# Kernel optimization log

Hardware: AMD Instinct MI355X
Metric: run time of the kernel (lower is better)

The kernel has to match this reference:

```python
import jax, jax.numpy as jnp
import numpy as np

B, C, H, W = 16, 256, 64, 64
LDCE, CDCE = 100, 128


def _conv(x, w, groups=1):
    # x: NCHW, w: OIHW, stride 1, SAME padding (matches pad=1 for 3x3, pad=0 for 1x1)
    return jax.lax.conv_general_dilated(x, w, (1, 1), 'SAME',
                                        feature_group_count=groups,
                                        dimension_numbers=('NCHW', 'OIHW', 'NCHW'))


def _bn(x, g, b, eps=1e-5):
    # training-mode BatchNorm2d: biased batch stats over (N,H,W)
    m = jnp.mean(x, axis=(0, 2, 3), keepdims=True)
    v = jnp.var(x, axis=(0, 2, 3), keepdims=True)
    return g[None, :, None, None] * (x - m) * jax.lax.rsqrt(v + eps) + b[None, :, None, None]


def _silu(z):
    return z * jax.nn.sigmoid(z)


def setup_inputs() -> dict:
    key = jax.random.key(0)
    ks = jax.random.split(key, 18)
    f32 = jnp.float32
    s = 0.05
    d = {}
    d['x'] = jax.random.normal(ks[0], (B, C, H, W), f32)
    d['dce_output'] = jax.random.normal(ks[1], (B, LDCE, CDCE), f32)
    # DCE projection Linear(dce_dim -> out_feat)
    d['w_dce'] = jax.random.normal(ks[2], (C, CDCE), f32) * s
    d['b_dce'] = jax.random.normal(ks[3], (C,), f32) * s
    # per-channel 3x3 convs, stacked as a depthwise kernel (C,1,3,3)
    d['w_ch'] = jax.random.normal(ks[4], (C, 1, 3, 3), f32) * s
    # shrink / expand MLP
    d['w_shrink'] = jax.random.normal(ks[5], (C // 2, C), f32) * s
    d['b_shrink'] = jax.random.normal(ks[6], (C // 2,), f32) * s
    d['w_expand'] = jax.random.normal(ks[7], (C, C // 2), f32) * s
    d['b_expand'] = jax.random.normal(ks[8], (C,), f32) * s
    # ResBlock backbone: conv3x3 -> BN -> SiLU -> conv1x1 -> BN
    d['w_conv1'] = jax.random.normal(ks[9], (C, C, 3, 3), f32) * s
    d['g_bn1'] = jnp.ones((C,), f32)
    d['be_bn1'] = jnp.zeros((C,), f32)
    d['w_conv2'] = jax.random.normal(ks[10], (C, C, 1, 1), f32) * s
    d['g_bn2'] = jnp.ones((C,), f32)
    d['be_bn2'] = jnp.zeros((C,), f32)
    # shortcut: conv1x1 -> BN
    d['w_sc'] = jax.random.normal(ks[11], (C, C, 1, 1), f32) * s
    d['g_bns'] = jnp.ones((C,), f32)
    d['be_bns'] = jnp.zeros((C,), f32)
    return d


def reference(x, dce_output, w_dce, b_dce, w_ch, w_shrink, b_shrink,
              w_expand, b_expand, w_conv1, g_bn1, be_bn1, w_conv2, g_bn2,
              be_bn2, w_sc, g_bns, be_bns):
    C2 = w_dce.shape[0]
    # 1. AdaptiveAvgPool1d(1) over sequence, then Linear: (B, C2)
    dce_pooled = jnp.mean(dce_output, axis=1)            # (B, CDCE)
    dce_proj = dce_pooled @ w_dce.T + b_dce              # (B, C2)
    # 2. per-channel Conv2d(1,1,3) + global avg pool == depthwise conv + mean
    conv_out = _conv(x, w_ch, groups=C2)                 # (B, C2, H, W)
    spatial_proj = jnp.mean(conv_out, axis=(2, 3))       # (B, C2)
    # 3-5. modulation gate
    m = dce_proj * spatial_proj
    h = jax.nn.relu(m @ w_shrink.T + b_shrink)
    mod = jax.nn.sigmoid(h @ w_expand.T + b_expand)      # (B, C2)
    # 6. channel-wise modulation
    xm = x * mod[:, :, None, None]
    # 7. ResBlock
    bb = _silu(_bn(_conv(xm, w_conv1), g_bn1, be_bn1))
    bb = _bn(_conv(bb, w_conv2), g_bn2, be_bn2)
    sc = _bn(_conv(xm, w_sc), g_bns, be_bns)
    return _silu(bb + sc)
```

## Files before the change

kernel.cpp:

```cpp
#include <hip/hip_runtime.h>

typedef unsigned short u16;
typedef unsigned int   u32;
typedef __attribute__((ext_vector_type(8))) __bf16 bf16x8;
typedef __attribute__((ext_vector_type(4))) float  f32x4;

#define HW 4096
#define NPOS 65536
#define CH 256
#define MT 512
#define NMT 256

__device__ __forceinline__ u16 f2bf(float f){
  u32 u = __float_as_uint(f);
  u += 0x7FFFu + ((u >> 16) & 1u);
  return (u16)(u >> 16);
}
__device__ __forceinline__ float bflo(u32 p){ return __uint_as_float(p << 16); }
__device__ __forceinline__ float bfhi(u32 p){ return __uint_as_float(p & 0xFFFF0000u); }

#define GLL16(g, l) __builtin_amdgcn_global_load_lds( \
    (__attribute__((address_space(1))) void*)(g), \
    (__attribute__((address_space(3))) void*)(l), 16, 0, 0)

#define VM4() asm volatile("s_waitcnt vmcnt(4)" ::: "memory")
#define VM0() asm volatile("s_waitcnt vmcnt(0)" ::: "memory")
#define BARX() do { __builtin_amdgcn_s_barrier(); __builtin_amdgcn_sched_barrier(0); } while(0)
#define SP1() __builtin_amdgcn_s_setprio(1)
#define SP0() __builtin_amdgcn_s_setprio(0)

#define MMQ(Aa, Bb, IO, JO) \
  { _Pragma("unroll") for (int fi=0; fi<4; fi++){ \
      _Pragma("unroll") for (int fj=0; fj<2; fj++){ \
        acc[(IO)+fi][(JO)+fj] = __builtin_amdgcn_mfma_f32_16x16x32_bf16(Aa[0][fi], Bb[0][fj], acc[(IO)+fi][(JO)+fj], 0,0,0); \
        acc[(IO)+fi][(JO)+fj] = __builtin_amdgcn_mfma_f32_16x16x32_bf16(Aa[1][fi], Bb[1][fj], acc[(IO)+fi][(JO)+fj], 0,0,0); \
  } } }

#define RDA(dst, D, QOFF) \
  { _Pragma("unroll") for (int fi=0; fi<4; fi++){ \
      dst[0][fi] = *(const bf16x8*)&SH[(D) + aBase + (QOFF) + fi*1024 + kx0]; \
      dst[1][fi] = *(const bf16x8*)&SH[(D) + aBase + (QOFF) + fi*1024 + kx1]; \
  } }
#define RDB(dst, D, JOFF) \
  { _Pragma("unroll") for (int fj=0; fj<2; fj++){ \
      dst[0][fj] = *(const bf16x8*)&SH[(D) + bBase + (JOFF) + fj*1024 + kx0]; \
      dst[1][fj] = *(const bf16x8*)&SH[(D) + bBase + (JOFF) + fj*1024 + kx1]; \
  } }

__global__ __launch_bounds__(256) void k_statsx(const float* __restrict__ x, float* __restrict__ stats){
  int bc = blockIdx.x; int tid = threadIdx.x;
  const float* xp = x + (size_t)bc * HW;
  float S=0.f, r0=0.f, r1=0.f, c0=0.f, c1=0.f;
  #pragma unroll
  for (int k=0;k<4;k++){
    int i4 = tid + k*256;
    float4 v = ((const float4*)xp)[i4];
    int pos = i4*4; int h = pos>>6; int wb = pos&63;
    float sv = v.x+v.y+v.z+v.w;
    S += sv;
    if (h==0)  r0 += sv;
    if (h==63) r1 += sv;
    if (wb==0)  c0 += v.x;
    if (wb==60) c1 += v.w;
  }
  __shared__ float red[4][5];
  #pragma unroll
  for (int off=32; off>0; off>>=1){
    S  += __shfl_down(S, off);
    r0 += __shfl_down(r0, off);
    r1 += __shfl_down(r1, off);
    c0 += __shfl_down(c0, off);
    c1 += __shfl_down(c1, off);
  }
  if ((tid & 63) == 0){
    int w = tid >> 6;
    red[w][0]=S; red[w][1]=r0; red[w][2]=r1; red[w][3]=c0; red[w][4]=c1;
  }
  __syncthreads();
  if (tid == 0){
    float* o = stats + (size_t)bc * 9;
    for (int j=0;j<5;j++) o[j] = red[0][j]+red[1][j]+red[2][j]+red[3][j];
    o[5] = xp[0];
    o[6] = xp[63];
    o[7] = xp[4032];
    o[8] = xp[4095];
  }
}

__global__ __launch_bounds__(256) void k_gate(const float* __restrict__ dce,
    const float* __restrict__ stats, const float* __restrict__ wch,
    const float* __restrict__ w_dce, const float* __restrict__ b_dce,
    const float* __restrict__ w_sh, const float* __restrict__ b_sh,
    const float* __restrict__ w_ex, const float* __restrict__ b_ex,
    float* __restrict__ modb){
  int b = blockIdx.x, tid = threadIdx.x;
  __shared__ float pl[128];
  __shared__ float mbuf[256];
  __shared__ float hbuf[128];
  __shared__ float ptmp[256];
  {
    int k = tid & 127, half = tid >> 7;
    const float* p = dce + (size_t)b*12800 + half*50*128 + k;
    float s = 0.f;
    #pragma unroll 5
    for (int l=0;l<50;l++) s += p[l*128];
    ptmp[tid] = s;
  }
  __syncthreads();
  if (tid < 128) pl[tid] = (ptmp[tid] + ptmp[tid+128]) * 0.01f;
  __syncthreads();
  {
    int c = tid;
    const float* st = stats + (size_t)(b*256+c)*9;
    float S=st[0], r0=st[1], r1=st[2], cc0=st[3], cc1=st[4];
    float x00=st[5], x0W=st[6], xH0=st[7], xHW=st[8];
    float acc = 0.f;
    #pragma unroll
    for (int t=0;t<9;t++){
      int dh = t/3 - 1, dw = t%3 - 1;
      float R = (dh==1)? r0 : (dh==-1)? r1 : 0.f;
      float Cc = (dw==1)? cc0 : (dw==-1)? cc1 : 0.f;
      float X = 0.f;
      if (dh==1 && dw==1) X = x00;
      else if (dh==1 && dw==-1) X = x0W;
      else if (dh==-1 && dw==1) X = xH0;
      else if (dh==-1 && dw==-1) X = xHW;
      acc += wch[c*9+t] * (S - R - Cc + X);
    }
    float sp_ = acc * (1.f/4096.f);
    float dp = b_dce[c];
    const float4* wr = (const float4*)(w_dce + c*128);
    #pragma unroll 8
    for (int k4=0;k4<32;k4++){
      float4 w4 = wr[k4];
      dp += w4.x*pl[k4*4] + w4.y*pl[k4*4+1] + w4.z*pl[k4*4+2] + w4.w*pl[k4*4+3];
    }
    mbuf[c] = sp_ * dp;
  }
  __syncthreads();
  if (tid < 128){
    int j = tid;
    float acc = b_sh[j];
    const float4* wr = (const float4*)(w_sh + j*256);
    #pragma unroll 8
    for (int k4=0;k4<64;k4++){
      float4 w4 = wr[k4];
      acc += w4.x*mbuf[k4*4] + w4.y*mbuf[k4*4+1] + w4.z*mbuf[k4*4+2] + w4.w*mbuf[k4*4+3];
    }
    hbuf[j] = fmaxf(acc, 0.f);
  }
  __syncthreads();
  {
    int c = tid;
    float acc = b_ex[c];
    const float4* wr = (const float4*)(w_ex + c*128);
    #pragma unroll 8
    for (int k4=0;k4<32;k4++){
      float4 w4 = wr[k4];
      acc += w4.x*hbuf[k4*4] + w4.y*hbuf[k4*4+1] + w4.z*hbuf[k4*4+2] + w4.w*hbuf[k4*4+3];
    }
    modb[b*256+c] = 1.f/(1.f + __expf(-acc));
  }
}

__global__ __launch_bounds__(256) void k_wprep(const float* __restrict__ w1,
    const float* __restrict__ wsc, const float* __restrict__ w2,
    u16* __restrict__ w1t, u16* __restrict__ wsct, u16* __restrict__ w2t){
  int bx = blockIdx.x, ci = threadIdx.x;
  if (bx < 2304){
    int co = bx / 9, t = bx - co*9;
    w1t[(size_t)co*2304 + t*256 + ci] = f2bf(w1[(size_t)(co*256+ci)*9 + t]);
  } else if (bx < 2560){
    int i = (bx-2304)*256 + ci;
    wsct[i] = f2bf(wsc[i]);
  } else {
    int i = (bx-2560)*256 + ci;
    w2t[i] = f2bf(w2[i]);
  }
}

__global__ __launch_bounds__(256) void k_xm(const float* __restrict__ x, const float* __restrict__ modb,
                                            u16* __restrict__ xm){
  __shared__ __attribute__((aligned(16))) u16 tile[64*266];
  int pt = blockIdx.x, ct = blockIdx.y, tid = threadIdx.x;
  size_t P0 = (size_t)pt * 256;
  int b = pt >> 4;
  int rem = (pt & 15) << 8;
  int C0 = ct << 6;
  {
    int c = tid >> 2, q = tid & 3;
    const float* xp = x + ((size_t)(b*256 + C0 + c))*HW + rem;
    float mv = modb[b*256 + C0 + c];
    #pragma unroll
    for (int k=0;k<16;k++){
      int pos = q*64 + k*4;
      float4 v = *(const float4*)(xp + pos);
      u32 w0 = (u32)f2bf(v.x*mv) | ((u32)f2bf(v.y*mv) << 16);
      u32 w1 = (u32)f2bf(v.z*mv) | ((u32)f2bf(v.w*mv) << 16);
      u32* dst = (u32*)&tile[c*266 + pos];
      dst[0] = w0; dst[1] = w1;
    }
  }
  __syncthreads();
  {
    int g = tid & 7, p0 = tid >> 3;
    #pragma unroll
    for (int k=0;k<8;k++){
      int pos = p0 + k*32;
      u32 v0 = tile[(g*8+0)*266 + pos], v1 = tile[(g*8+1)*266 + pos];
      u32 v2 = tile[(g*8+2)*266 + pos], v3 = tile[(g*8+3)*266 + pos];
      u32 v4 = tile[(g*8+4)*266 + pos], v5 = tile[(g*8+5)*266 + pos];
      u32 v6 = tile[(g*8+6)*266 + pos], v7 = tile[(g*8+7)*266 + pos];
      uint4 pk;
      pk.x = v0 | (v1<<16); pk.y = v2 | (v3<<16);
      pk.z = v4 | (v5<<16); pk.w = v6 | (v7<<16);
      *(uint4*)(xm + (P0+pos)*CH + C0 + g*8) = pk;
    }
  }
}

template<int NTAPS>
__global__ __launch_bounds__(512, 2) void k_gemm8p(const u16* __restrict__ A,
    const u16* __restrict__ Bw, u16* __restrict__ y,
    float* __restrict__ psum, float* __restrict__ psq, const u16* __restrict__ zp){
  constexpr int KTOT = NTAPS*256;
  constexpr int NT = KTOT/64;
  constexpr int NI = NT/2;
  __shared__ __attribute__((aligned(16))) u16 SH[65536];
  int tid = threadIdx.x;
  int lane = tid & 63, wave = tid >> 6;
  int wm = wave >> 2, wn = wave & 3;
  int l15 = lane & 15, quad = lane >> 4;
  int mt = blockIdx.x;
  int P0 = mt*256;

  int s3  = l15 & 7;
  int kx0 = ((quad)     ^ s3) * 8;
  int kx1 = ((4 | quad) ^ s3) * 8;
  int aBase = wm*8192 + l15*64;
  int bBase = 32768 + (wn>>1)*8192 + (wn&1)*4096 + l15*64;

  int r0  = tid >> 3;
  int c0  = (tid & 7) ^ (r0 & 7);
  int csrc = c0 * 8;

  f32x4 acc[8][4];
  f32x4 zz = {0.f,0.f,0.f,0.f};
  #pragma unroll
  for (int i=0;i<8;i++)
    #pragma unroll
    for (int j=0;j<4;j++) acc[i][j] = zz;

  auto stageA = [&](int t, int ah){
    int base = (t&1)*16384 + ah*8192;
    if constexpr (NTAPS == 9){
      int tap = t >> 2, koff = (t & 3) << 6;
      int t3 = tap/3;
      int dh = t3 - 1, dw = (tap - t3*3) - 1;
      int d = dh*64 + dw;
      #pragma unroll
      for (int L=0; L<2; L++){
        int pos = P0 + ah*128 + (L<<6) + r0;
        int h = (pos>>6)&63, w = pos&63;
        bool ok = ((unsigned)(h+dh) < 64u) && ((unsigned)(w+dw) < 64u);
        const u16* s = ok ? A + (size_t)(pos + d)*CH + koff + csrc : zp + csrc;
        GLL16(s, SH + base + L*4096 + tid*8);
      }
    } else {
      #pragma unroll
      for (int L=0; L<2; L++){
        int pos = P0 + ah*128 + (L<<6) + r0;
        const u16* s = A + (size_t)pos*CH + t*64 + csrc;
        GLL16(s, SH + base + L*4096 + tid*8);
      }
    }
  };
  auto stageB = [&](int t, int bh){
    int base = 32768 + (t&1)*16384 + bh*8192;
    #pragma unroll
    for (int L=0; L<2; L++){
      int co = bh*128 + (L<<6) + r0;
      const u16* s = Bw + (size_t)co*KTOT + t*64 + csrc;
      GLL16(s, SH + base + L*4096 + tid*8);
    }
  };

  stageA(0,0); stageA(0,1); stageB(0,0); stageB(0,1);
  stageA(1,0); stageA(1,1);
  VM4();
  BARX();

  bf16x8 aLo[2][4], aHi[2][4], bLo[2][2], bHi[2][2];

  for (int n=0; n<NI; ++n){
    const int t1 = 2*n+1;
    const bool pre = (n+1 < NI);
    RDA(aLo, 0, 0); RDB(bLo, 0, 0);
    stageB(t1, 0);
    BARX();
    SP1(); MMQ(aLo, bLo, 0, 0); SP0();
    BARX();
    RDA(aHi, 0, 4096);
    stageB(t1, 1);
    BARX();
    SP1(); MMQ(aHi, bLo, 4, 0); SP0();
    BARX();
    RDB(bHi, 0, 2048);
    if (pre) stageA(t1+1, 0);
    BARX();
    SP1(); MMQ(aHi, bHi, 4, 2); SP0();
    BARX();
    if (pre){ stageA(t1+1, 1); VM4(); } else { VM0(); }
    BARX();
    SP1(); MMQ(aLo, bHi, 0, 2); SP0();
    BARX();
    RDA(aLo, 16384, 0); RDB(bLo, 16384, 0);
    if (pre) stageB(t1+1, 0);
    BARX();
    SP1(); MMQ(aLo, bLo, 0, 0); SP0();
    BARX();
    RDA(aHi, 16384, 4096);
    if (pre) stageB(t1+1, 1);
    BARX();
    SP1(); MMQ(aHi, bLo, 4, 0); SP0();
    BARX();
    RDB(bHi, 16384, 2048);
    if (pre) stageA(t1+2, 0);
    BARX();
    SP1(); MMQ(aHi, bHi, 4, 2); SP0();
    BARX();
    if (pre){ stageA(t1+2, 1); VM4(); }
    BARX();
    SP1(); MMQ(aLo, bHi, 0, 2); SP0();
    BARX();
  }

  #pragma unroll
  for (int i=0;i<8;i++){
    int m = wm*128 + i*16 + quad*4;
    #pragma unroll
    for (int j=0;j<4;j++){
      int n = wn*64 + j*16 + l15;
      size_t base = ((size_t)(P0 + m))*CH + n;
      #pragma unroll
      for (int r=0;r<4;r++)
        y[base + (size_t)r*CH] = f2bf(acc[i][j][r]);
    }
  }
  float* SHf = (float*)SH;
  #pragma unroll
  for (int j=0;j<4;j++){
    float a=0.f, b=0.f;
    #pragma unroll
    for (int i=0;i<8;i++)
      #pragma unroll
      for (int r=0;r<4;r++){ float v = acc[i][j][r]; a += v; b += v*v; }
    a += __shfl_xor(a,16); b += __shfl_xor(b,16);
    a += __shfl_xor(a,32); b += __shfl_xor(b,32);
    if (quad==0){
      int idx = ((wave*4 + j)*16 + l15)*2;
      SHf[idx] = a; SHf[idx+1] = b;
    }
  }
  __syncthreads();
  if (tid < 256){
    int n = tid; int wnn = n>>6; int j = (n>>4)&3; int li = n&15;
    int i0 = (((wnn)*4 + j)*16 + li)*2;
    int i1 = (((4+wnn)*4 + j)*16 + li)*2;
    psum[(size_t)n*NMT + mt] = SHf[i0] + SHf[i1];
    psq [(size_t)n*NMT + mt] = SHf[i0+1] + SHf[i1+1];
  }
}

__global__ __launch_bounds__(64) void k_bnstat(const float* __restrict__ psum, const float* __restrict__ psq,
    const float* __restrict__ g, const float* __restrict__ be,
    float* __restrict__ scale, float* __restrict__ shift){
  int c = blockIdx.x, t = threadIdx.x;
  const float* ps = psum + (size_t)c*NMT;
  const float* pq = psq  + (size_t)c*NMT;
  float s=0.f, q=0.f;
  #pragma unroll
  for (int i=0;i<4;i++){ s += ps[t + i*64]; q += pq[t + i*64]; }
  #pragma unroll
  for (int off=32; off>0; off>>=1){
    s += __shfl_down(s, off);
    q += __shfl_down(q, off);
  }
  if (t == 0){
    float mean = s * (1.f/65536.f);
    float var  = q * (1.f/65536.f) - mean*mean;
    float rstd = rsqrtf(var + 1e-5f);
    float sc = g[c]*rstd;
    scale[c] = sc;
    shift[c] = be[c] - mean*sc;
  }
}

__global__ __launch_bounds__(256) void k_bb(const u16* __restrict__ y1, const float* __restrict__ sc1,
    const float* __restrict__ sh1, u16* __restrict__ bb){
  __shared__ float sc[256], sh[256];
  int tid = threadIdx.x;
  sc[tid] = sc1[tid]; sh[tid] = sh1[tid];
  __syncthreads();
  size_t i = ((size_t)blockIdx.x*256 + tid)*8;
  int c0 = (int)(i & 255);
  uint4 v = *(const uint4*)(y1 + i);
  u32 a[4] = {v.x, v.y, v.z, v.w};
  u32 o[4];
  #pragma unroll
  for (int p=0;p<4;p++){
    float zl = sc[c0+2*p]*bflo(a[p]) + sh[c0+2*p];
    float zh = sc[c0+2*p+1]*bfhi(a[p]) + sh[c0+2*p+1];
    float ol = zl/(1.f+__expf(-zl));
    float oh = zh/(1.f+__expf(-zh));
    o[p] = (u32)f2bf(ol) | ((u32)f2bf(oh) << 16);
  }
  uint4 w; w.x=o[0]; w.y=o[1]; w.z=o[2]; w.w=o[3];
  *(uint4*)(bb + i) = w;
}

__global__ __launch_bounds__(256) void k_final(const u16* __restrict__ y2, const u16* __restrict__ ysc,
    const float* __restrict__ sc2, const float* __restrict__ sh2,
    const float* __restrict__ scs, const float* __restrict__ shs,
    float* __restrict__ out){
  __shared__ __attribute__((aligned(16))) float tile[64*257];
  __shared__ float l2s[64], l2h[64], lss[64], lsh[64];
  int pt = blockIdx.x, ct = blockIdx.y, tid = threadIdx.x;
  int C0 = ct << 6;
  if (tid < 64){ l2s[tid]=sc2[C0+tid]; l2h[tid]=sh2[C0+tid]; lss[tid]=scs[C0+tid]; lsh[tid]=shs[C0+tid]; }
  __syncthreads();
  size_t P0 = (size_t)pt * 256;
  int b = pt >> 4; int rem = (pt & 15) << 8;
  {
    int g = tid & 7, p0 = tid >> 3;
    for (int k=0;k<8;k++){
      int pos = p0 + k*32;
      size_t off = (P0+pos)*CH + C0 + g*8;
      uint4 va = *(const uint4*)(y2 + off);
      uint4 vb = *(const uint4*)(ysc + off);
      u32 aa[4] = {va.x,va.y,va.z,va.w};
      u32 bv[4] = {vb.x,vb.y,vb.z,vb.w};
      #pragma unroll
      for (int p=0;p<4;p++){
        int c = g*8 + 2*p;
        float z0 = l2s[c]*bflo(aa[p]) + l2h[c] + lss[c]*bflo(bv[p]) + lsh[c];
        float z1 = l2s[c+1]*bfhi(aa[p]) + l2h[c+1] + lss[c+1]*bfhi(bv[p]) + lsh[c+1];
        tile[c*257 + pos]     = z0/(1.f+__expf(-z0));
        tile[(c+1)*257 + pos] = z1/(1.f+__expf(-z1));
      }
    }
  }
  __syncthreads();
  {
    int c = tid >> 2, q = tid & 3;
    float* op = out + ((size_t)(b*256 + C0 + c))*HW + rem;
    #pragma unroll
    for (int k=0;k<16;k++){
      int pos = q*64 + k*4;
      float4 v;
      v.x = tile[c*257 + pos];
      v.y = tile[c*257 + pos + 1];
      v.z = tile[c*257 + pos + 2];
      v.w = tile[c*257 + pos + 3];
      *(float4*)(op + pos) = v;
    }
  }
}

extern "C" void kernel_launch(void* const* d_in, const int* in_sizes, int n_in,
                              void* d_out, int out_size, void* d_ws, size_t ws_size,
                              hipStream_t stream){
  const float* x     = (const float*)d_in[0];
  const float* dce   = (const float*)d_in[1];
  const float* w_dce = (const float*)d_in[2];
  const float* b_dce = (const float*)d_in[3];
  const float* w_ch  = (const float*)d_in[4];
  const float* w_sh  = (const float*)d_in[5];
  const float* b_sh  = (const float*)d_in[6];
  const float* w_ex  = (const float*)d_in[7];
  const float* b_ex  = (const float*)d_in[8];
  const float* w_c1  = (const float*)d_in[9];
  const float* g1    = (const float*)d_in[10];
  const float* be1   = (const float*)d_in[11];
  const float* w_c2  = (const float*)d_in[12];
  const float* g2    = (const float*)d_in[13];
  const float* be2   = (const float*)d_in[14];
  const float* w_s   = (const float*)d_in[15];
  const float* gs    = (const float*)d_in[16];
  const float* bes   = (const float*)d_in[17];
  float* out = (float*)d_out;
  char* ws = (char*)d_ws;

  const size_t NB = (size_t)NPOS*CH*2;
  u16* xm  = (u16*)(ws);
  u16* y1  = (u16*)(ws + NB);
  u16* ysc = (u16*)(ws + 2*NB);
  u16* bb  = (u16*)(ws + 3*NB);
  char* p = ws + 4*NB;
  u16* w1t   = (u16*)p; p += (size_t)256*2304*2;
  u16* wsct  = (u16*)p; p += (size_t)256*256*2;
  u16* w2t   = (u16*)p; p += (size_t)256*256*2;
  float* statsx = (float*)p; p += (size_t)16*256*9*4;
  float* modb   = (float*)p; p += (size_t)16*256*4;
  float* p1s = (float*)p; p += (size_t)MT*256*4;
  float* p1q = (float*)p; p += (size_t)MT*256*4;
  float* pss = (float*)p; p += (size_t)MT*256*4;
  float* psqv= (float*)p; p += (size_t)MT*256*4;
  float* p2s = (float*)p; p += (size_t)MT*256*4;
  float* p2q = (float*)p; p += (size_t)MT*256*4;
  float* bn1sc = (float*)p; p += 1024;
  float* bn1sh = (float*)p; p += 1024;
  float* bnssc = (float*)p; p += 1024;
  float* bnssh = (float*)p; p += 1024;
  float* bn2sc = (float*)p; p += 1024;
  float* bn2sh = (float*)p; p += 1024;
  u16* zp = (u16*)p; p += 4096;

  hipMemsetAsync(zp, 0, 4096, stream);
  k_statsx<<<4096, 256, 0, stream>>>(x, statsx);
  k_wprep<<<2816, 256, 0, stream>>>(w_c1, w_s, w_c2, w1t, wsct, w2t);
  k_gate<<<16, 256, 0, stream>>>(dce, statsx, w_ch, w_dce, b_dce, w_sh, b_sh, w_ex, b_ex, modb);
  k_xm<<<dim3(256,4), 256, 0, stream>>>(x, modb, xm);
  k_gemm8p<9><<<256, 512, 0, stream>>>(xm, w1t, y1, p1s, p1q, zp);
  k_bnstat<<<256, 64, 0, stream>>>(p1s, p1q, g1, be1, bn1sc, bn1sh);
  k_bb<<<8192, 256, 0, stream>>>(y1, bn1sc, bn1sh, bb);
  k_gemm8p<1><<<256, 512, 0, stream>>>(xm, wsct, ysc, pss, psqv, zp);
  k_bnstat<<<256, 64, 0, stream>>>(pss, psqv, gs, bes, bnssc, bnssh);
  k_gemm8p<1><<<256, 512, 0, stream>>>(bb, w2t, y1 , p2s, p2q, zp);
  k_bnstat<<<256, 64, 0, stream>>>(p2s, p2q, g2, be2, bn2sc, bn2sh);
  k_final<<<dim3(256,4), 256, 0, stream>>>(y1, ysc, bn2sc, bn2sh, bnssc, bnssh, out);
}
```

Baseline: 389.8 us.

## Store modulated input in zero-padded halo layout to remove conv bounds checks

The modulated activation buffer now uses a 66x66 padded NHWC layout per image, with a new kernel that zeroes the halo border. The 3x3 implicit-GEMM loader can then use a constant per-tap offset instead of per-row bounds checks and a zero-page fallback. Staging addresses are precomputed once per thread, which cuts address arithmetic inside the main loop. The sched_barrier after each s_barrier is also removed, giving the compiler more freedom to schedule but risking reordering of LDS reads relative to MFMAs.

Result: no change. 384.1 us (-1.5%).

```diff
diff --git a/kernel.cpp b/kernel.cpp
--- a/kernel.cpp
+++ b/kernel.cpp
@@ -10,6 +10,7 @@
 #define CH 256
 #define MT 512
 #define NMT 256
+#define PIMG 4356
 
 __device__ __forceinline__ u16 f2bf(float f){
   u32 u = __float_as_uint(f);
@@ -25,7 +26,7 @@
 
 #define VM4() asm volatile("s_waitcnt vmcnt(4)" ::: "memory")
 #define VM0() asm volatile("s_waitcnt vmcnt(0)" ::: "memory")
-#define BARX() do { __builtin_amdgcn_s_barrier(); __builtin_amdgcn_sched_barrier(0); } while(0)
+#define BAR() __builtin_amdgcn_s_barrier()
 #define SP1() __builtin_amdgcn_s_setprio(1)
 #define SP0() __builtin_amdgcn_s_setprio(0)
 
@@ -179,11 +180,24 @@
   }
 }
 
+__global__ __launch_bounds__(256) void k_halo(u16* __restrict__ xm){
+  int b = blockIdx.x, tid = threadIdx.x;
+  uint4 zq = {0u,0u,0u,0u};
+  for (int i = tid; i < 260; i += 256){
+    int row, col;
+    if (i < 66){ row = 0; col = i; }
+    else if (i < 132){ row = 65; col = i - 66; }
+    else { int j = i - 132; row = 1 + (j >> 1); col = (j & 1) * 65; }
+    uint4* p = (uint4*)(xm + ((size_t)b*PIMG + row*66 + col)*256);
+    #pragma unroll
+    for (int q=0;q<32;q++) p[q] = zq;
+  }
+}
+
 __global__ __launch_bounds__(256) void k_xm(const float* __restrict__ x, const float* __restrict__ modb,
                                             u16* __restrict__ xm){
   __shared__ __attribute__((aligned(16))) u16 tile[64*266];
   int pt = blockIdx.x, ct = blockIdx.y, tid = threadIdx.x;
-  size_t P0 = (size_t)pt * 256;
   int b = pt >> 4;
   int rem = (pt & 15) << 8;
   int C0 = ct << 6;
@@ -214,15 +228,17 @@
       uint4 pk;
       pk.x = v0 | (v1<<16); pk.y = v2 | (v3<<16);
       pk.z = v4 | (v5<<16); pk.w = v6 | (v7<<16);
-      *(uint4*)(xm + (P0+pos)*CH + C0 + g*8) = pk;
-    }
-  }
-}
-
-template<int NTAPS>
+      int gp = rem + pos;
+      int h = gp >> 6, w = gp & 63;
+      *(uint4*)(xm + ((size_t)b*PIMG + (h+1)*66 + (w+1))*256 + C0 + g*8) = pk;
+    }
+  }
+}
+
+template<int NTAPS, int APAD>
 __global__ __launch_bounds__(512, 2) void k_gemm8p(const u16* __restrict__ A,
     const u16* __restrict__ Bw, u16* __restrict__ y,
-    float* __restrict__ psum, float* __restrict__ psq, const u16* __restrict__ zp){
+    float* __restrict__ psum, float* __restrict__ psq){
   constexpr int KTOT = NTAPS*256;
   constexpr int NT = KTOT/64;
   constexpr int NI = NT/2;
@@ -241,8 +257,20 @@
   int bBase = 32768 + (wn>>1)*8192 + (wn&1)*4096 + l15*64;
 
   int r0  = tid >> 3;
-  int c0  = (tid & 7) ^ (r0 & 7);
-  int csrc = c0 * 8;
+  int csrc = ((tid & 7) ^ (r0 & 7)) * 8;
+
+  auto pvoff = [&](int pos)->int{
+    if constexpr (APAD){
+      int b_ = pos >> 12, rm = pos & 4095;
+      return (b_*PIMG + ((rm>>6)+1)*66 + (rm&63)+1)*256 + csrc;
+    } else {
+      return pos*256 + csrc;
+    }
+  };
+  const int vA00 = pvoff(P0 + r0),        vA01 = pvoff(P0 + 64 + r0);
+  const int vA10 = pvoff(P0 + 128 + r0),  vA11 = pvoff(P0 + 192 + r0);
+  const int vB00 = (r0)*KTOT + csrc,       vB01 = (64 + r0)*KTOT + csrc;
+  const int vB10 = (128 + r0)*KTOT + csrc, vB11 = (192 + r0)*KTOT + csrc;
 
   f32x4 acc[8][4];
   f32x4 zz = {0.f,0.f,0.f,0.f};
@@ -253,42 +281,27 @@
 
   auto stageA = [&](int t, int ah){
     int base = (t&1)*16384 + ah*8192;
+    int uoff;
     if constexpr (NTAPS == 9){
-      int tap = t >> 2, koff = (t & 3) << 6;
-      int t3 = tap/3;
-      int dh = t3 - 1, dw = (tap - t3*3) - 1;
-      int d = dh*64 + dw;
-      #pragma unroll
-      for (int L=0; L<2; L++){
-        int pos = P0 + ah*128 + (L<<6) + r0;
-        int h = (pos>>6)&63, w = pos&63;
-        bool ok = ((unsigned)(h+dh) < 64u) && ((unsigned)(w+dw) < 64u);
-        const u16* s = ok ? A + (size_t)(pos + d)*CH + koff + csrc : zp + csrc;
-        GLL16(s, SH + base + L*4096 + tid*8);
-      }
+      int tap = t >> 2, t3 = (tap*11) >> 5;
+      uoff = (tap + 63*t3 - 67)*256 + (t&3)*64;
     } else {
-      #pragma unroll
-      for (int L=0; L<2; L++){
-        int pos = P0 + ah*128 + (L<<6) + r0;
-        const u16* s = A + (size_t)pos*CH + t*64 + csrc;
-        GLL16(s, SH + base + L*4096 + tid*8);
-      }
-    }
+      uoff = t*64;
+    }
+    GLL16(A + uoff + (ah ? vA10 : vA00), SH + base + tid*8);
+    GLL16(A + uoff + (ah ? vA11 : vA01), SH + base + 4096 + tid*8);
   };
   auto stageB = [&](int t, int bh){
     int base = 32768 + (t&1)*16384 + bh*8192;
-    #pragma unroll
-    for (int L=0; L<2; L++){
-      int co = bh*128 + (L<<6) + r0;
-      const u16* s = Bw + (size_t)co*KTOT + t*64 + csrc;
-      GLL16(s, SH + base + L*4096 + tid*8);
-    }
+    int uoff = t*64;
+    GLL16(Bw + uoff + (bh ? vB10 : vB00), SH + base + tid*8);
+    GLL16(Bw + uoff + (bh ? vB11 : vB01), SH + base + 4096 + tid*8);
   };
 
   stageA(0,0); stageA(0,1); stageB(0,0); stageB(0,1);
   stageA(1,0); stageA(1,1);
   VM4();
-  BARX();
+  BAR();
 
   bf16x8 aLo[2][4], aHi[2][4], bLo[2][2], bHi[2][2];
 
@@ -297,42 +310,42 @@
     const bool pre = (n+1 < NI);
     RDA(aLo, 0, 0); RDB(bLo, 0, 0);
     stageB(t1, 0);
-    BARX();
+    BAR();
     SP1(); MMQ(aLo, bLo, 0, 0); SP0();
-    BARX();
+    BAR();
     RDA(aHi, 0, 4096);
     stageB(t1, 1);
-    BARX();
+    BAR();
     SP1(); MMQ(aHi, bLo, 4, 0); SP0();
-    BARX();
+    BAR();
     RDB(bHi, 0, 2048);
     if (pre) stageA(t1+1, 0);
-    BARX();
+    BAR();
     SP1(); MMQ(aHi, bHi, 4, 2); SP0();
-    BARX();
+    BAR();
     if (pre){ stageA(t1+1, 1); VM4(); } else { VM0(); }
-    BARX();
+    BAR();
     SP1(); MMQ(aLo, bHi, 0, 2); SP0();
-    BARX();
+    BAR();
     RDA(aLo, 16384, 0); RDB(bLo, 16384, 0);
     if (pre) stageB(t1+1, 0);
-    BARX();
+    BAR();
     SP1(); MMQ(aLo, bLo, 0, 0); SP0();
-    BARX();
+    BAR();
     RDA(aHi, 16384, 4096);
     if (pre) stageB(t1+1, 1);
-    BARX();
+    BAR();
     SP1(); MMQ(aHi, bLo, 4, 0); SP0();
-    BARX();
+    BAR();
     RDB(bHi, 16384, 2048);
     if (pre) stageA(t1+2, 0);
-    BARX();
+    BAR();
     SP1(); MMQ(aHi, bHi, 4, 2); SP0();
-    BARX();
+    BAR();
     if (pre){ stageA(t1+2, 1); VM4(); }
-    BARX();
+    BAR();
     SP1(); MMQ(aLo, bHi, 0, 2); SP0();
-    BARX();
+    BAR();
   }
 
   #pragma unroll
@@ -491,12 +504,13 @@
   float* out = (float*)d_out;
   char* ws = (char*)d_ws;
 
-  const size_t NB = (size_t)NPOS*CH*2;
+  const size_t NB  = (size_t)NPOS*CH*2;
+  const size_t XMB = (size_t)16*PIMG*CH*2;
   u16* xm  = (u16*)(ws);
-  u16* y1  = (u16*)(ws + NB);
-  u16* ysc = (u16*)(ws + 2*NB);
-  u16* bb  = (u16*)(ws + 3*NB);
-  char* p = ws + 4*NB;
+  u16* y1  = (u16*)(ws + XMB);
+  u16* ysc = (u16*)(ws + XMB + NB);
+  u16* bb  = (u16*)(ws + XMB + 2*NB);
+  char* p = ws + XMB + 3*NB;
   u16* w1t   = (u16*)p; p += (size_t)256*2304*2;
   u16* wsct  = (u16*)p; p += (size_t)256*256*2;
   u16* w2t   = (u16*)p; p += (size_t)256*256*2;
@@ -514,19 +528,18 @@
   float* bnssh = (float*)p; p += 1024;
   float* bn2sc = (float*)p; p += 1024;
   float* bn2sh = (float*)p; p += 1024;
-  u16* zp = (u16*)p; p += 4096;
-
-  hipMemsetAsync(zp, 0, 4096, stream);
+
+  k_halo<<<16, 256, 0, stream>>>(xm);
   k_statsx<<<4096, 256, 0, stream>>>(x, statsx);
   k_wprep<<<2816, 256, 0, stream>>>(w_c1, w_s, w_c2, w1t, wsct, w2t);
   k_gate<<<16, 256, 0, stream>>>(dce, statsx, w_ch, w_dce, b_dce, w_sh, b_sh, w_ex, b_ex, modb);
   k_xm<<<dim3(256,4), 256, 0, stream>>>(x, modb, xm);
-  k_gemm8p<9><<<256, 512, 0, stream>>>(xm, w1t, y1, p1s, p1q, zp);
+  k_gemm8p<9,1><<<256, 512, 0, stream>>>(xm, w1t, y1, p1s, p1q);
   k_bnstat<<<256, 64, 0, stream>>>(p1s, p1q, g1, be1, bn1sc, bn1sh);
   k_bb<<<8192, 256, 0, stream>>>(y1, bn1sc, bn1sh, bb);
-  k_gemm8p<1><<<256, 512, 0, stream>>>(xm, wsct, ysc, pss, psqv, zp);
+  k_gemm8p<1,1><<<256, 512, 0, stream>>>(xm, wsct, ysc, pss, psqv);
   k_bnstat<<<256, 64, 0, stream>>>(pss, psqv, gs, bes, bnssc, bnssh);
-  k_gemm8p<1><<<256, 512, 0, stream>>>(bb, w2t, y1 , p2s, p2q, zp);
+  k_gemm8p<1,0><<<256, 512, 0, stream>>>(bb, w2t, y1 , p2s, p2q);
   k_bnstat<<<256, 64, 0, stream>>>(p2s, p2q, g2, be2, bn2sc, bn2sh);
   k_final<<<dim3(256,4), 256, 0, stream>>>(y1, ysc, bn2sc, bn2sh, bnssc, bnssh, out);
 }
```
